# Kernel optimization log

Measured on AMD Instinct MI355X. Metric: run time of the kernel, lower is better.

## Reference

```python
import jax, jax.numpy as jnp
import numpy as np

# ---- config constants (match init_kwargs / MjModel camera params) ----
PAD_RES = (255, 255)          # padded sensor resolution (Mx, My), odd
RES = (160, 160)              # eye resolution (target_width, target_height)
APERTURE = 0.1                # aperture as fraction of sensor half-size
WAVELENGTHS = (6.1e-07, 5.3e-07, 4.7e-07)  # RGB wavelengths [m]
SENSOR_SIZE = (2e-3, 2e-3)    # (sx, sy) from MjModel.cam_sensorsize [m]


def setup_inputs() -> dict:
    key = jax.random.key(0)
    k1, k2 = jax.random.split(key)
    image = jax.random.uniform(k1, (PAD_RES[0], PAD_RES[1], 3), dtype=jnp.float32)
    depth = jax.random.uniform(k2, (PAD_RES[0], PAD_RES[1]), dtype=jnp.float32)
    return {"image": image, "depth": depth}


def _optics_consts():
    """Precompute the grids of MjCambrianOptics._reset_psf."""
    Mx, My = PAD_RES
    sx, sy = SENSOR_SIZE
    dx, dy = sx / Mx, sy / My
    Lx, Ly = dx * Mx, dy * My
    x1 = jnp.linspace(-Lx / 2.0, Lx / 2.0, Mx, dtype=jnp.float32)
    y1 = jnp.linspace(-Ly / 2.0, Ly / 2.0, My, dtype=jnp.float32)
    X1, Y1 = jnp.meshgrid(x1, y1, indexing='ij')
    fx = jnp.linspace(-1.0 / (2.0 * dx), 1.0 / (2.0 * dx), Mx, dtype=jnp.float32)
    fy = jnp.linspace(-1.0 / (2.0 * dx), 1.0 / (2.0 * dx), My, dtype=jnp.float32)  # dx for both, faithful to source
    FX, FY = jnp.meshgrid(fx, fy, indexing='ij')
    aperture_radius = min(Lx / 2, Ly / 2) * APERTURE + 1e-07
    A = (jnp.sqrt(X1**2 + Y1**2) / aperture_radius <= 1.0).astype(jnp.float32)
    wl = jnp.asarray(WAVELENGTHS, dtype=jnp.float32)[:, None, None]  # (3,1,1)
    X1_Y1 = X1**2 + Y1**2                                           # (Mx,My)
    H_valid = (jnp.sqrt(FX**2 + FY**2) < 1.0 / wl).astype(jnp.float32)  # (3,Mx,My)
    arg = 1.0 - (wl * FX) ** 2 - (wl * FY) ** 2
    # Source computes sqrt(arg) (NaN where arg<0) then nan_to_num after exp;
    # H_valid is exactly 0 where arg<=0, so clamping arg to 0 yields the same H.
    FX_FY = jnp.sqrt(jnp.maximum(arg, 0.0))                         # (3,Mx,My)
    k = (1j * 2.0 * jnp.pi / wl).astype(jnp.complex64)              # (3,1,1)
    return A, X1_Y1, H_valid, FX_FY, k


def _depth_invariant_psf(mean_depth):
    A, X1_Y1, H_valid, FX_FY, k = _optics_consts()
    # spherical wave from point source at mean_depth, masked by aperture
    u1 = jnp.exp(k * jnp.sqrt(X1_Y1 + mean_depth**2))   # (3,Mx,My) complex64
    u2 = u1 * A
    # angular-spectrum transfer function
    H = H_valid * jnp.exp(k * mean_depth * FX_FY)
    u3 = jnp.fft.ifft2(jnp.fft.fft2(H) * jnp.fft.fft2(u2))
    psf = u3 * u3                                        # complex square, faithful to torch.square
    psf = psf / (jnp.sum(psf) + 1e-07)                   # complex normalization, faithful
    return jnp.real(psf)                                 # (3,Mx,My) float32


def reference(image, depth):
    psf = _depth_invariant_psf(jnp.mean(depth))          # (3,Mx,My)
    img = jnp.transpose(image, (2, 0, 1))[None]          # (1,3,H,W)
    kern = psf[:, None].astype(img.dtype)                # (3,1,Mx,My)
    out = jax.lax.conv_general_dilated(
        img, kern, window_strides=(1, 1), padding='SAME',
        feature_group_count=3, dimension_numbers=('NCHW', 'OIHW', 'NCHW'))
    out = jnp.transpose(out[0], (1, 2, 0))               # (H,W,3)
    width, height = out.shape[0], out.shape[1]
    target_width, target_height = RES
    top = (height - target_height) // 2
    left = (width - target_width) // 2
    out = out[top:top + target_height, left:left + target_width]
    return jnp.clip(out, 0.0, 1.0)
```

## Files before the change

kernel.cpp:

```cpp
#include <hip/hip_runtime.h>
#include <hip/hip_bf16.h>
#include <math.h>


constexpr int M   = 255;
constexpr int NP  = M * M;
constexpr int RESO = 160;

constexpr int IMG_ROWS = 416, IMG_COLS = 448;
constexpr int IMG_CH   = IMG_ROWS * IMG_COLS;
constexpr int IMG_SIDE = 3 * IMG_CH;
constexpr int P4_DI   = 304 * 8;
constexpr int P4_CH   = 256 * P4_DI;
constexpr int P4_SIDE = 3 * P4_CH;

typedef __attribute__((ext_vector_type(8))) short short8;
typedef __attribute__((ext_vector_type(4))) float f32x4;

__device__ __forceinline__ unsigned short f2bf(float f) {
    unsigned int u = __float_as_uint(f);
    unsigned int r = (u + 0x7fffu + ((u >> 16) & 1u)) >> 16;
    return (unsigned short)r;
}
__device__ __forceinline__ float bf2f(unsigned short h) {
    return __uint_as_float(((unsigned int)h) << 16);
}

constexpr int MAXN = 1100;
struct PWForest {
    int kind[MAXN];
    int off[MAXN], len[MAXN];
    int li[MAXN], ri[MAXN];
    int lvl[MAXN];
    int nNode, nLeaf, maxLvl;
    int roots[16], nRoots;
};
constexpr int pwf_build(PWForest& T, int o, int n) {
    if (n <= 128) {
        int id = T.nNode++;
        T.kind[id] = 0; T.off[id] = o; T.len[id] = n;
        T.lvl[id] = 0; T.nLeaf++;
        return id;
    }
    int n2 = (n / 2) - ((n / 2) % 8);
    int a = pwf_build(T, o, n2);
    int b = pwf_build(T, o + n2, n - n2);
    int id = T.nNode++;
    T.kind[id] = 1; T.li[id] = a; T.ri[id] = b;
    int l = (T.lvl[a] > T.lvl[b] ? T.lvl[a] : T.lvl[b]) + 1;
    T.lvl[id] = l; if (l > T.maxLvl) T.maxLvl = l;
    return id;
}
constexpr PWForest pwf_make() {
    PWForest T{};
    int pos = 1, rem = NP - 1;
    while (rem > 0) {
        int c = rem > 8192 ? 8192 : rem;
        T.roots[T.nRoots++] = pwf_build(T, pos, c);
        pos += c; rem -= c;
    }
    return T;
}
constexpr PWForest PW = pwf_make();
static_assert(PW.nNode <= MAXN, "forest overflow");
static_assert(PW.nRoots == 8, "chunk count");

__global__ void k_mleaf(const float* __restrict__ depth, float* __restrict__ val) {
    int id = blockIdx.x * 256 + threadIdx.x;
    if (id >= PW.nNode || PW.kind[id] != 0) return;
    const float* a = depth + PW.off[id];
    int n = PW.len[id];
    float r0 = a[0], r1 = a[1], r2 = a[2], r3 = a[3];
    float r4 = a[4], r5 = a[5], r6 = a[6], r7 = a[7];
    int lim = n - (n % 8);
    int i = 8;
    for (; i < lim; i += 8) {
        r0 += a[i + 0]; r1 += a[i + 1]; r2 += a[i + 2]; r3 += a[i + 3];
        r4 += a[i + 4]; r5 += a[i + 5]; r6 += a[i + 6]; r7 += a[i + 7];
    }
    float res = ((r0 + r1) + (r2 + r3)) + ((r4 + r5) + (r6 + r7));
    for (; i < n; ++i) res += a[i];
    val[id] = res;
}

__global__ void k_mtree(const float* __restrict__ depth, float* __restrict__ val,
                        float* __restrict__ meanp) {
    int tid = threadIdx.x;
    for (int l = 1; l <= PW.maxLvl; ++l) {
        for (int id = tid; id < PW.nNode; id += 256)
            if (PW.kind[id] == 1 && PW.lvl[id] == l)
                val[id] = val[PW.li[id]] + val[PW.ri[id]];
        __syncthreads();
    }
    if (tid == 0) {
        float io1 = depth[0];
        for (int r = 0; r < PW.nRoots; ++r)
            io1 = io1 + val[PW.roots[r]];
        meanp[0] = io1 / 65025.0f;
    }
}

__global__ void k_prep(const float* __restrict__ img, unsigned short* __restrict__ IMG2,
                       float2* __restrict__ W,
                       float2* __restrict__ U2, float2* __restrict__ Hb,
                       const float* __restrict__ meanp,
                       double xstart, double xstep, double xstop,
                       double fstart, double fstep, double fstop,
                       float ap_f) {
#pragma clang fp contract(off)
    int idx = blockIdx.x * 256 + threadIdx.x;
    if (idx < 3 * NP) {
        int c = idx / NP, ij = idx % NP, i = ij / M, j = ij % M;
        const float wls[3] = {6.1e-07f, 5.3e-07f, 4.7e-07f};
        float wl = wls[c];
        float ki = ((float)6.283185307179586) / wl;
        float d  = meanp[0];
        float d2 = d * d;

        float x  = (i == 254) ? (float)xstop : (float)((double)i * xstep + xstart);
        float y  = (j == 254) ? (float)xstop : (float)((double)j * xstep + xstart);
        float fx = (i == 254) ? (float)fstop : (float)((double)i * fstep + fstart);
        float fy = (j == 254) ? (float)fstop : (float)((double)j * fstep + fstart);

        float xx = x * x, yy = y * y;
        float X1Y1 = xx + yy;

        float s  = sqrtf(X1Y1 + d2);
        float th = ki * s;
        float A  = (sqrtf(X1Y1) / ap_f <= 1.0f) ? 1.0f : 0.0f;
        float2 u2v;
        if (A != 0.0f) u2v = make_float2((float)cos((double)th), (float)sin((double)th));
        else           u2v = make_float2(0.0f, 0.0f);

        float a = wl * fx, b = wl * fy;
        float arg = (1.0f - a * a) - b * b;
        float FXY = sqrtf(fmaxf(arg, 0.0f));
        float Hv  = (sqrtf(fx * fx + fy * fy) < (1.0f / wl)) ? 1.0f : 0.0f;
        float kd  = ki * d;
        float ph  = kd * FXY;
        float cph = (float)cos((double)ph), sph = (float)sin((double)ph);
        float2 hv = make_float2(Hv * cph, Hv * sph);

        U2[idx] = u2v;
        Hb[idx] = hv;
        return;
    }
    if (idx < 4 * NP) {
        int e = idx - 3 * NP;
        int n = e / M, k = e % M;
        int m = (n * k) % M;
        double ang = -2.0 * 3.14159265358979323846 * (double)m / 255.0;
        W[e] = make_float2((float)cos(ang), (float)sin(ang));
        return;
    }
    int e = idx - 4 * NP;
    if (e >= IMG_SIDE) return;
    int ch = e / IMG_CH, rem = e % IMG_CH;
    int prow = rem / IMG_COLS, pcol = rem % IMG_COLS;
    int a = prow - 80, b = pcol - 80;
    float v = 0.0f;
    if (a >= 0 && a < M && b >= 0 && b < M) v = img[(a * M + b) * 3 + ch];
    unsigned short hi = f2bf(v);
    unsigned short lo = f2bf(v - bf2f(hi));
    IMG2[e] = hi;
    IMG2[IMG_SIDE + e] = lo;
}

#define CG_LOAD(KT, VA, WB0, WB1) { \
    int k0_ = (KT) * 16; \
    { int r_ = threadIdx.x >> 4, c_ = threadIdx.x & 15; \
      int gi_ = i0 + r_, gk_ = k0_ + c_; \
      VA = (gi_ < M && gk_ < M) ? Ab[gi_ * M + gk_] : make_float2(0.f, 0.f); \
      if (conjA) VA.y = -VA.y; } \
    { int r2_ = threadIdx.x >> 5, c2_ = threadIdx.x & 31; \
      int gk2_ = k0_ + r2_, gj_ = j0 + c2_; \
      WB0 = make_float2(0.f, 0.f); \
      if (gk2_ < M && gj_ < M) { \
          WB0 = Bb[gk2_ * M + gj_]; \
          if (B2b) { float2 z_ = B2b[gk2_ * M + gj_]; \
              WB0 = make_float2(WB0.x * z_.x - WB0.y * z_.y, WB0.x * z_.y + WB0.y * z_.x); } \
      } \
      if (conjB) WB0.y = -WB0.y; } \
    { int idx_ = threadIdx.x + 256; \
      int r2_ = idx_ >> 5, c2_ = idx_ & 31; \
      int gk2_ = k0_ + r2_, gj_ = j0 + c2_; \
      WB1 = make_float2(0.f, 0.f); \
      if (gk2_ < M && gj_ < M) { \
          WB1 = Bb[gk2_ * M + gj_]; \
          if (B2b) { float2 z_ = B2b[gk2_ * M + gj_]; \
              WB1 = make_float2(WB1.x * z_.x - WB1.y * z_.y, WB1.x * z_.y + WB1.y * z_.x); } \
      } \
      if (conjB) WB1.y = -WB1.y; } }

__global__ __launch_bounds__(256)
void k_cgemm(const float2* __restrict__ A, int aBatch,
             const float2* __restrict__ B, const float2* __restrict__ B2,
             int bBatch, float2* __restrict__ C,
             int conjA, int conjB, float scale) {
    __shared__ float2 As[16][17];
    __shared__ float2 Bs[16][33];
    int c = blockIdx.z;
    int tx = threadIdx.x & 15, ty = threadIdx.x >> 4;
    int i0 = blockIdx.y * 16, j0 = blockIdx.x * 32;
    const float2* Ab = A + (size_t)c * aBatch;
    const float2* Bb = B + (size_t)c * bBatch;
    const float2* B2b = B2 ? (B2 + (size_t)c * bBatch) : nullptr;
    float2 a00 = {0,0}, a01 = {0,0};

    int wrA  = threadIdx.x >> 4,  wcA  = threadIdx.x & 15;
    int wrB0 = threadIdx.x >> 5,  wcB0 = threadIdx.x & 31;
    int wrB1 = (threadIdx.x + 256) >> 5, wcB1 = (threadIdx.x + 256) & 31;

    float2 vA, wB0, wB1;
    float2 nA, nB0, nB1;
    CG_LOAD(0, vA, wB0, wB1)

    for (int kt = 0; kt < 16; ++kt) {
        As[wrA][wcA]   = vA;
        Bs[wrB0][wcB0] = wB0;
        Bs[wrB1][wcB1] = wB1;
        if (kt < 15) { CG_LOAD(kt + 1, nA, nB0, nB1) }
        __syncthreads();
#pragma unroll
        for (int kk = 0; kk < 16; ++kk) {
            float2 p = As[ty][kk];
            float2 u = Bs[kk][tx], v = Bs[kk][tx + 16];
            a00.x += p.x * u.x - p.y * u.y;  a00.y += p.x * u.y + p.y * u.x;
            a01.x += p.x * v.x - p.y * v.y;  a01.y += p.x * v.y + p.y * v.x;
        }
        __syncthreads();
        vA = nA; wB0 = nB0; wB1 = nB1;
    }
    float2* Cb = C + (size_t)c * NP;
    int gi  = i0 + ty;
    int gj0 = j0 + tx, gj1 = j0 + tx + 16;
    if (gi < M && gj0 < M) Cb[gi * M + gj0] = make_float2(a00.x * scale, a00.y * scale);
    if (gi < M && gj1 < M) Cb[gi * M + gj1] = make_float2(a01.x * scale, a01.y * scale);
}

__global__ void k_sred(const float2* __restrict__ U3, double2* __restrict__ spart) {
    __shared__ double sx[256], sy[256];
    int t = threadIdx.x;
    double ax = 0.0, ay = 0.0;
    for (int i = blockIdx.x * 256 + t; i < 3 * NP; i += 64 * 256) {
        double zx = (double)U3[i].x, zy = (double)U3[i].y;
        ax += zx * zx - zy * zy;
        ay += 2.0 * zx * zy;
    }
    sx[t] = ax; sy[t] = ay;
    __syncthreads();
    for (int w = 128; w > 0; w >>= 1) {
        if (t < w) { sx[t] += sx[t + w]; sy[t] += sy[t + w]; }
        __syncthreads();
    }
    if (t == 0) spart[blockIdx.x] = make_double2(sx[0], sy[0]);
}

__global__ void k_sfin(const double2* __restrict__ spart, double* __restrict__ sfin) {
    if (threadIdx.x != 0 || blockIdx.x != 0) return;
    double rx = 0.0, ry = 0.0;
    for (int i = 0; i < 64; ++i) { rx += spart[i].x; ry += spart[i].y; }
    double dsx = rx + 1e-7, dsy = ry;
    sfin[0] = dsx;
    sfin[1] = dsy;
    sfin[2] = 1.0 / (dsx * dsx + dsy * dsy);
}

__global__ void k_p4(const float2* __restrict__ U3, const double* __restrict__ sfin,
                     unsigned short* __restrict__ P4) {
    int idx = blockIdx.x * 256 + threadIdx.x;
    if (idx >= P4_SIDE) return;
    double dsx = sfin[0], dsy = sfin[1], inv = sfin[2];
    int ch = idx / P4_CH, rem = idx % P4_CH;
    int di = rem / P4_DI, rem2 = rem % P4_DI;
    int u = rem2 / 8, t = rem2 % 8;
    int p = u - 16 + t;
    float v = 0.0f;
    if (di < M && p >= 0 && p < M) {
        float2 zf = U3[(ch * M + di) * M + p];
        double zx = (double)zf.x, zy = (double)zf.y;
        double zr = zx * zx - zy * zy;
        double zi = 2.0 * zx * zy;
        v = (float)((zr * dsx + zi * dsy) * inv);
    }
    unsigned short hi = f2bf(v);
    unsigned short lo = f2bf(v - bf2f(hi));
    P4[idx] = hi;
    P4[P4_SIDE + idx] = lo;
}

constexpr int LDS_STRIDE = 312;

#define SB __builtin_amdgcn_sched_barrier(0);

#define REP9(OP) OP(0) OP(1) OP(2) OP(3) OP(4) OP(5) OP(6) OP(7) OP(8)

#define DECLA(i) short8 Ah_##i, Al_##i;
#define DECLB(i) short8 Bh_##i, Bl_##i;

#define LDA(i) Ah_##i = *(const short8*)(prH + 256 * i); \
               Al_##i = *(const short8*)(prL + 256 * i);
#define LDB(i) Bh_##i = *(const short8*)(prH + 256 * i); \
               Bl_##i = *(const short8*)(prL + 256 * i);
#define LOADA(dl) { const unsigned short* prH = pHc + (size_t)(d0 + (dl)) * P4_DI + aoff; \
                    const unsigned short* prL = pLc + (size_t)(d0 + (dl)) * P4_DI + aoff; \
                    REP9(LDA) }
#define LOADB(dl) { const unsigned short* prH = pHc + (size_t)(d0 + (dl)) * P4_DI + aoff; \
                    const unsigned short* prL = pLc + (size_t)(d0 + (dl)) * P4_DI + aoff; \
                    REP9(LDB) }

#define CMA(i) { \
    short8 bh0 = *(const short8*)&ldsI[0][rrow][32 * i + 8 * q]; \
    short8 bl0 = *(const short8*)&ldsI[1][rrow][32 * i + 8 * q]; \
    short8 bh1 = *(const short8*)&ldsI[0][rrow][32 * i + 8 * q + 16]; \
    short8 bl1 = *(const short8*)&ldsI[1][rrow][32 * i + 8 * q + 16]; \
    aHH0 = __builtin_amdgcn_mfma_f32_16x16x32_bf16(Ah_##i, bh0, aHH0, 0, 0, 0); \
    aHL0 = __builtin_amdgcn_mfma_f32_16x16x32_bf16(Ah_##i, bl0, aHL0, 0, 0, 0); \
    aLH0 = __builtin_amdgcn_mfma_f32_16x16x32_bf16(Al_##i, bh0, aLH0, 0, 0, 0); \
    aHH1 = __builtin_amdgcn_mfma_f32_16x16x32_bf16(Ah_##i, bh1, aHH1, 0, 0, 0); \
    aHL1 = __builtin_amdgcn_mfma_f32_16x16x32_bf16(Ah_##i, bl1, aHL1, 0, 0, 0); \
    aLH1 = __builtin_amdgcn_mfma_f32_16x16x32_bf16(Al_##i, bh1, aLH1, 0, 0, 0); }
#define CMB(i) { \
    short8 bh0 = *(const short8*)&ldsI[0][rrow][32 * i + 8 * q]; \
    short8 bl0 = *(const short8*)&ldsI[1][rrow][32 * i + 8 * q]; \
    short8 bh1 = *(const short8*)&ldsI[0][rrow][32 * i + 8 * q + 16]; \
    short8 bl1 = *(const short8*)&ldsI[1][rrow][32 * i + 8 * q + 16]; \
    aHH0 = __builtin_amdgcn_mfma_f32_16x16x32_bf16(Bh_##i, bh0, aHH0, 0, 0, 0); \
    aHL0 = __builtin_amdgcn_mfma_f32_16x16x32_bf16(Bh_##i, bl0, aHL0, 0, 0, 0); \
    aLH0 = __builtin_amdgcn_mfma_f32_16x16x32_bf16(Bl_##i, bh0, aLH0, 0, 0, 0); \
    aHH1 = __builtin_amdgcn_mfma_f32_16x16x32_bf16(Bh_##i, bh1, aHH1, 0, 0, 0); \
    aHL1 = __builtin_amdgcn_mfma_f32_16x16x32_bf16(Bh_##i, bl1, aHL1, 0, 0, 0); \
    aLH1 = __builtin_amdgcn_mfma_f32_16x16x32_bf16(Bl_##i, bh1, aLH1, 0, 0, 0); }
#define COMPA(dl) { int rrow = ln + (dl); REP9(CMA) }
#define COMPB(dl) { int rrow = ln + (dl); REP9(CMB) }

__global__ __launch_bounds__(256, 2)
void k_conv(const unsigned short* __restrict__ IMG2,
            const unsigned short* __restrict__ P4,
            float* __restrict__ PART) {
    __shared__ __align__(16) unsigned short ldsI[2][31][LDS_STRIDE];

    int tid  = threadIdx.x;
    int w    = tid >> 6;
    int lane = tid & 63;
    int ln   = lane & 15;
    int q    = lane >> 4;
    int j0 = blockIdx.x * 32;
    int i0 = blockIdx.y * 16;
    int bz = blockIdx.z;
    int ch = bz >> 4, chunk = bz & 15;
    int d0 = chunk << 4;

    const unsigned short* imgH = IMG2 + ch * IMG_CH;
    const unsigned short* imgL = imgH + IMG_SIDE;
    const unsigned short* pHc  = P4 + ch * P4_CH;
    const unsigned short* pLc  = pHc + P4_SIDE;

    int su0  = 16 + 8 * q - ln;
    int aoff = su0 * 8;

    f32x4 aHH0 = {0.f,0.f,0.f,0.f}, aHL0 = {0.f,0.f,0.f,0.f}, aLH0 = {0.f,0.f,0.f,0.f};
    f32x4 aHH1 = {0.f,0.f,0.f,0.f}, aHL1 = {0.f,0.f,0.f,0.f}, aLH1 = {0.f,0.f,0.f,0.f};

    REP9(DECLA)
    REP9(DECLB)

    int dbase = 4 * w;
    LOADA(dbase + 0)

    int row0 = i0 + d0;
    for (int idx = tid; idx < 2 * 31 * 38; idx += 256) {
        int plane = idx / (31 * 38);
        int rem = idx - plane * (31 * 38);
        int r = rem / 38, c = rem - r * 38;
        const unsigned short* src =
            (plane ? imgL : imgH) + (size_t)(row0 + r) * IMG_COLS + j0 + c * 8;
        *(short8*)&ldsI[plane][r][c * 8] = *(const short8*)src;
    }
    __syncthreads();

    LOADB(dbase + 1)
    SB
    COMPA(dbase + 0)
    SB
    LOADA(dbase + 2)
    SB
    COMPB(dbase + 1)
    SB
    LOADB(dbase + 3)
    SB
    COMPA(dbase + 2)
    SB
    COMPB(dbase + 3)

    f32x4 tot0, tot1;
#pragma unroll
    for (int r = 0; r < 4; ++r) {
        tot0[r] = aHH0[r] + aHL0[r] + aLH0[r];
        tot1[r] = aHH1[r] + aHL1[r] + aLH1[r];
    }

    __syncthreads();
    float* red = (float*)&ldsI[0][0][0];
    if (w) {
#pragma unroll
        for (int r = 0; r < 4; ++r) {
            red[((w - 1) * 64 + lane) * 8 + r]     = tot0[r];
            red[((w - 1) * 64 + lane) * 8 + 4 + r] = tot1[r];
        }
    }
    __syncthreads();
    if (w == 0) {
#pragma unroll
        for (int wv = 0; wv < 3; ++wv)
#pragma unroll
            for (int r = 0; r < 4; ++r) {
                tot0[r] += red[(wv * 64 + lane) * 8 + r];
                tot1[r] += red[(wv * 64 + lane) * 8 + 4 + r];
            }
        float* op = PART + (size_t)bz * (RESO * RESO) + (i0 + ln) * RESO + j0 + 4 * q;
        float4 o0; o0.x = tot0[0]; o0.y = tot0[1]; o0.z = tot0[2]; o0.w = tot0[3];
        float4 o1; o1.x = tot1[0]; o1.y = tot1[1]; o1.z = tot1[2]; o1.w = tot1[3];
        *(float4*)op = o0;
        *(float4*)(op + 16) = o1;
    }
}

__global__ void k_out(const float* __restrict__ PART, float* __restrict__ out) {
    int idx = blockIdx.x * 256 + threadIdx.x;
    if (idx >= 3 * RESO * RESO) return;
    int c = idx / (RESO * RESO), ij = idx % (RESO * RESO);
    float s = 0.0f;
    for (int kz = 0; kz < 16; ++kz)
        s += PART[(size_t)(c * 16 + kz) * (RESO * RESO) + ij];
    s = fminf(fmaxf(s, 0.0f), 1.0f);
    int i = ij / RESO, j = ij % RESO;
    out[(i * RESO + j) * 3 + c] = s;
}

extern "C" void kernel_launch(void* const* d_in, const int* in_sizes, int n_in,
                              void* d_out, int out_size, void* d_ws, size_t ws_size,
                              hipStream_t stream) {
    const float* image = (const float*)d_in[0];
    const float* depth = (const float*)d_in[1];
    float* out = (float*)d_out;

    char* p = (char*)d_ws;
    auto alloc = [&](size_t bytes) { void* r = (void*)p; p += (bytes + 255) & ~(size_t)255; return r; };
    float*   meanp = (float*)alloc(4);
    float*   mval  = (float*)alloc(MAXN * 4);
    double*  sfin  = (double*)alloc(3 * 8);
    float2*  Wf    = (float2*)alloc((size_t)NP * 8);
    float2*  UH    = (float2*)alloc((size_t)6 * NP * 8);
    float2*  Td    = (float2*)alloc((size_t)6 * NP * 8);
    float2*  EF    = (float2*)alloc((size_t)6 * NP * 8);
    float2*  U3    = (float2*)alloc((size_t)3 * NP * 8);
    double2* spart = (double2*)alloc(64 * 16);
    unsigned short* P4   = (unsigned short*)alloc((size_t)2 * P4_SIDE * 2);
    unsigned short* IMG2 = (unsigned short*)alloc((size_t)2 * IMG_SIDE * 2);
    float*   PART  = (float*)alloc((size_t)48 * RESO * RESO * 4);

    float2* U2 = UH;
    float2* Hb = UH + (size_t)3 * NP;

    double dx = 0.002 / 255.0;
    double Lx = dx * 255.0;
    double ap = (Lx / 2.0) * 0.1 + 1e-7;
    float ap_f = (float)ap;

    double xstart = -(Lx / 2.0);
    double xstop  =  Lx / 2.0;
    double xstep  = (xstop - xstart) / 254.0;
    double fstart = -1.0 / (2.0 * dx);
    double fstop  =  1.0 / (2.0 * dx);
    double fstep  = (fstop - fstart) / 254.0;

    k_mleaf<<<(PW.nNode + 255) / 256, 256, 0, stream>>>(depth, mval);
    k_mtree<<<1, 256, 0, stream>>>(depth, mval, meanp);
    int gprep = (4 * NP + IMG_SIDE + 255) / 256;
    k_prep<<<gprep, 256, 0, stream>>>(image, IMG2, Wf, U2, Hb, meanp,
                                      xstart, xstep, xstop,
                                      fstart, fstep, fstop, ap_f);

    dim3 bb(256);
    k_cgemm<<<dim3(8, 16, 6), bb, 0, stream>>>(Wf, 0, UH, nullptr, NP, Td, 0, 0, 1.0f);
    k_cgemm<<<dim3(8, 16, 6), bb, 0, stream>>>(Td, NP, Wf, nullptr, 0, EF, 0, 0, 1.0f);
    k_cgemm<<<dim3(8, 16, 3), bb, 0, stream>>>(Wf, 0, EF + (size_t)3 * NP, EF, NP,
                                               Td, 1, 0, 1.0f / 255.0f);
    k_cgemm<<<dim3(8, 16, 3), bb, 0, stream>>>(Td, NP, Wf, nullptr, 0, U3, 0, 1,
                                               1.0f / 255.0f);

    k_sred<<<64, 256, 0, stream>>>(U3, spart);
    k_sfin<<<1, 64, 0, stream>>>(spart, sfin);
    k_p4<<<(P4_SIDE + 255) / 256, 256, 0, stream>>>(U3, sfin, P4);

    k_conv<<<dim3(5, 10, 48), 256, 0, stream>>>(IMG2, P4, PART);
    k_out<<<300, 256, 0, stream>>>(PART, out);
}
```

Measured before the change: 252.7 us.

## Double conv output rows per block to reuse PSF A-fragments; fold sfin into k_p4

The convolution block now computes 32 output rows instead of 16, so each PSF fragment held in registers feeds twice as many MFMAs. This halves the P4 global loads per output and halves the grid in y, at the cost of more accumulator registers and a taller LDS image tile. Separately, the single-thread k_sfin kernel is removed: every k_p4 block now re-reduces the 64 partial sums in shared memory, trading a kernel launch for redundant tiny work per block.

```diff
diff --git a/kernel.cpp b/kernel.cpp
--- a/kernel.cpp
+++ b/kernel.cpp
@@ -256,21 +256,20 @@
     if (t == 0) spart[blockIdx.x] = make_double2(sx[0], sy[0]);
 }
 
-__global__ void k_sfin(const double2* __restrict__ spart, double* __restrict__ sfin) {
-    if (threadIdx.x != 0 || blockIdx.x != 0) return;
-    double rx = 0.0, ry = 0.0;
-    for (int i = 0; i < 64; ++i) { rx += spart[i].x; ry += spart[i].y; }
-    double dsx = rx + 1e-7, dsy = ry;
-    sfin[0] = dsx;
-    sfin[1] = dsy;
-    sfin[2] = 1.0 / (dsx * dsx + dsy * dsy);
-}
-
-__global__ void k_p4(const float2* __restrict__ U3, const double* __restrict__ sfin,
+__global__ void k_p4(const float2* __restrict__ U3, const double2* __restrict__ spart,
                      unsigned short* __restrict__ P4) {
+    __shared__ double sh[3];
+    if (threadIdx.x == 0) {
+        double rx = 0.0, ry = 0.0;
+        for (int i = 0; i < 64; ++i) { rx += spart[i].x; ry += spart[i].y; }
+        double dsx_ = rx + 1e-7, dsy_ = ry;
+        sh[0] = dsx_; sh[1] = dsy_;
+        sh[2] = 1.0 / (dsx_ * dsx_ + dsy_ * dsy_);
+    }
+    __syncthreads();
     int idx = blockIdx.x * 256 + threadIdx.x;
     if (idx >= P4_SIDE) return;
-    double dsx = sfin[0], dsy = sfin[1], inv = sfin[2];
+    double dsx = sh[0], dsy = sh[1], inv = sh[2];
     int ch = idx / P4_CH, rem = idx % P4_CH;
     int di = rem / P4_DI, rem2 = rem % P4_DI;
     int u = rem2 / 8, t = rem2 % 8;
@@ -309,28 +308,30 @@
                     const unsigned short* prL = pLc + (size_t)(d0 + (dl)) * P4_DI + aoff; \
                     REP9(LDB) }
 
-#define CMA(i) { \
-    short8 bh0 = *(const short8*)&ldsI[0][rrow][32 * i + 8 * q]; \
-    short8 bl0 = *(const short8*)&ldsI[1][rrow][32 * i + 8 * q]; \
-    short8 bh1 = *(const short8*)&ldsI[0][rrow][32 * i + 8 * q + 16]; \
-    short8 bl1 = *(const short8*)&ldsI[1][rrow][32 * i + 8 * q + 16]; \
-    aHH0 = __builtin_amdgcn_mfma_f32_16x16x32_bf16(Ah_##i, bh0, aHH0, 0, 0, 0); \
-    aHL0 = __builtin_amdgcn_mfma_f32_16x16x32_bf16(Ah_##i, bl0, aHL0, 0, 0, 0); \
-    aLH0 = __builtin_amdgcn_mfma_f32_16x16x32_bf16(Al_##i, bh0, aLH0, 0, 0, 0); \
-    aHH1 = __builtin_amdgcn_mfma_f32_16x16x32_bf16(Ah_##i, bh1, aHH1, 0, 0, 0); \
-    aHL1 = __builtin_amdgcn_mfma_f32_16x16x32_bf16(Ah_##i, bl1, aHL1, 0, 0, 0); \
-    aLH1 = __builtin_amdgcn_mfma_f32_16x16x32_bf16(Al_##i, bh1, aLH1, 0, 0, 0); }
-#define CMB(i) { \
-    short8 bh0 = *(const short8*)&ldsI[0][rrow][32 * i + 8 * q]; \
-    short8 bl0 = *(const short8*)&ldsI[1][rrow][32 * i + 8 * q]; \
-    short8 bh1 = *(const short8*)&ldsI[0][rrow][32 * i + 8 * q + 16]; \
-    short8 bl1 = *(const short8*)&ldsI[1][rrow][32 * i + 8 * q + 16]; \
-    aHH0 = __builtin_amdgcn_mfma_f32_16x16x32_bf16(Bh_##i, bh0, aHH0, 0, 0, 0); \
-    aHL0 = __builtin_amdgcn_mfma_f32_16x16x32_bf16(Bh_##i, bl0, aHL0, 0, 0, 0); \
-    aLH0 = __builtin_amdgcn_mfma_f32_16x16x32_bf16(Bl_##i, bh0, aLH0, 0, 0, 0); \
-    aHH1 = __builtin_amdgcn_mfma_f32_16x16x32_bf16(Bh_##i, bh1, aHH1, 0, 0, 0); \
-    aHL1 = __builtin_amdgcn_mfma_f32_16x16x32_bf16(Bh_##i, bl1, aHL1, 0, 0, 0); \
-    aLH1 = __builtin_amdgcn_mfma_f32_16x16x32_bf16(Bl_##i, bh1, aLH1, 0, 0, 0); }
+#define CMBODY(AH, AL) { \
+    short8 bh00 = *(const short8*)&ldsI[0][rrow][colb]; \
+    short8 bl00 = *(const short8*)&ldsI[1][rrow][colb]; \
+    short8 bh01 = *(const short8*)&ldsI[0][rrow][colb + 16]; \
+    short8 bl01 = *(const short8*)&ldsI[1][rrow][colb + 16]; \
+    short8 bh10 = *(const short8*)&ldsI[0][rrow + 16][colb]; \
+    short8 bl10 = *(const short8*)&ldsI[1][rrow + 16][colb]; \
+    short8 bh11 = *(const short8*)&ldsI[0][rrow + 16][colb + 16]; \
+    short8 bl11 = *(const short8*)&ldsI[1][rrow + 16][colb + 16]; \
+    aHH00 = __builtin_amdgcn_mfma_f32_16x16x32_bf16(AH, bh00, aHH00, 0, 0, 0); \
+    aHL00 = __builtin_amdgcn_mfma_f32_16x16x32_bf16(AH, bl00, aHL00, 0, 0, 0); \
+    aLH00 = __builtin_amdgcn_mfma_f32_16x16x32_bf16(AL, bh00, aLH00, 0, 0, 0); \
+    aHH01 = __builtin_amdgcn_mfma_f32_16x16x32_bf16(AH, bh01, aHH01, 0, 0, 0); \
+    aHL01 = __builtin_amdgcn_mfma_f32_16x16x32_bf16(AH, bl01, aHL01, 0, 0, 0); \
+    aLH01 = __builtin_amdgcn_mfma_f32_16x16x32_bf16(AL, bh01, aLH01, 0, 0, 0); \
+    aHH10 = __builtin_amdgcn_mfma_f32_16x16x32_bf16(AH, bh10, aHH10, 0, 0, 0); \
+    aHL10 = __builtin_amdgcn_mfma_f32_16x16x32_bf16(AH, bl10, aHL10, 0, 0, 0); \
+    aLH10 = __builtin_amdgcn_mfma_f32_16x16x32_bf16(AL, bh10, aLH10, 0, 0, 0); \
+    aHH11 = __builtin_amdgcn_mfma_f32_16x16x32_bf16(AH, bh11, aHH11, 0, 0, 0); \
+    aHL11 = __builtin_amdgcn_mfma_f32_16x16x32_bf16(AH, bl11, aHL11, 0, 0, 0); \
+    aLH11 = __builtin_amdgcn_mfma_f32_16x16x32_bf16(AL, bh11, aLH11, 0, 0, 0); }
+
+#define CMA(i) { int colb = 32 * i + 8 * q; CMBODY(Ah_##i, Al_##i) }
+#define CMB(i) { int colb = 32 * i + 8 * q; CMBODY(Bh_##i, Bl_##i) }
 #define COMPA(dl) { int rrow = ln + (dl); REP9(CMA) }
 #define COMPB(dl) { int rrow = ln + (dl); REP9(CMB) }
 
@@ -338,7 +339,7 @@
 void k_conv(const unsigned short* __restrict__ IMG2,
             const unsigned short* __restrict__ P4,
             float* __restrict__ PART) {
-    __shared__ __align__(16) unsigned short ldsI[2][31][LDS_STRIDE];
+    __shared__ __align__(16) unsigned short ldsI[2][47][LDS_STRIDE];
 
     int tid  = threadIdx.x;
     int w    = tid >> 6;
@@ -346,7 +347,7 @@
     int ln   = lane & 15;
     int q    = lane >> 4;
     int j0 = blockIdx.x * 32;
-    int i0 = blockIdx.y * 16;
+    int i0 = blockIdx.y * 32;
     int bz = blockIdx.z;
     int ch = bz >> 4, chunk = bz & 15;
     int d0 = chunk << 4;
@@ -359,8 +360,10 @@
     int su0  = 16 + 8 * q - ln;
     int aoff = su0 * 8;
 
-    f32x4 aHH0 = {0.f,0.f,0.f,0.f}, aHL0 = {0.f,0.f,0.f,0.f}, aLH0 = {0.f,0.f,0.f,0.f};
-    f32x4 aHH1 = {0.f,0.f,0.f,0.f}, aHL1 = {0.f,0.f,0.f,0.f}, aLH1 = {0.f,0.f,0.f,0.f};
+    f32x4 aHH00 = {0,0,0,0}, aHL00 = {0,0,0,0}, aLH00 = {0,0,0,0};
+    f32x4 aHH01 = {0,0,0,0}, aHL01 = {0,0,0,0}, aLH01 = {0,0,0,0};
+    f32x4 aHH10 = {0,0,0,0}, aHL10 = {0,0,0,0}, aLH10 = {0,0,0,0};
+    f32x4 aHH11 = {0,0,0,0}, aHL11 = {0,0,0,0}, aLH11 = {0,0,0,0};
 
     REP9(DECLA)
     REP9(DECLB)
@@ -369,9 +372,9 @@
     LOADA(dbase + 0)
 
     int row0 = i0 + d0;
-    for (int idx = tid; idx < 2 * 31 * 38; idx += 256) {
-        int plane = idx / (31 * 38);
-        int rem = idx - plane * (31 * 38);
+    for (int idx = tid; idx < 2 * 47 * 38; idx += 256) {
+        int plane = idx / (47 * 38);
+        int rem = idx - plane * (47 * 38);
         int r = rem / 38, c = rem - r * 38;
         const unsigned short* src =
             (plane ? imgL : imgH) + (size_t)(row0 + r) * IMG_COLS + j0 + c * 8;
@@ -393,11 +396,13 @@
     SB
     COMPB(dbase + 3)
 
-    f32x4 tot0, tot1;
+    f32x4 tot00, tot01, tot10, tot11;
 #pragma unroll
     for (int r = 0; r < 4; ++r) {
-        tot0[r] = aHH0[r] + aHL0[r] + aLH0[r];
-        tot1[r] = aHH1[r] + aHL1[r] + aLH1[r];
+        tot00[r] = aHH00[r] + aHL00[r] + aLH00[r];
+        tot01[r] = aHH01[r] + aHL01[r] + aLH01[r];
+        tot10[r] = aHH10[r] + aHL10[r] + aLH10[r];
+        tot11[r] = aHH11[r] + aHL11[r] + aLH11[r];
     }
 
     __syncthreads();
@@ -405,8 +410,11 @@
     if (w) {
 #pragma unroll
         for (int r = 0; r < 4; ++r) {
-            red[((w - 1) * 64 + lane) * 8 + r]     = tot0[r];
-            red[((w - 1) * 64 + lane) * 8 + 4 + r] = tot1[r];
+            int base = ((w - 1) * 64 + lane) * 16;
+            red[base + r]      = tot00[r];
+            red[base + 4 + r]  = tot01[r];
+            red[base + 8 + r]  = tot10[r];
+            red[base + 12 + r] = tot11[r];
         }
     }
     __syncthreads();
@@ -415,14 +423,23 @@
         for (int wv = 0; wv < 3; ++wv)
 #pragma unroll
             for (int r = 0; r < 4; ++r) {
-                tot0[r] += red[(wv * 64 + lane) * 8 + r];
-                tot1[r] += red[(wv * 64 + lane) * 8 + 4 + r];
+                int base = (wv * 64 + lane) * 16;
+                tot00[r] += red[base + r];
+                tot01[r] += red[base + 4 + r];
+                tot10[r] += red[base + 8 + r];
+                tot11[r] += red[base + 12 + r];
             }
-        float* op = PART + (size_t)bz * (RESO * RESO) + (i0 + ln) * RESO + j0 + 4 * q;
-        float4 o0; o0.x = tot0[0]; o0.y = tot0[1]; o0.z = tot0[2]; o0.w = tot0[3];
-        float4 o1; o1.x = tot1[0]; o1.y = tot1[1]; o1.z = tot1[2]; o1.w = tot1[3];
-        *(float4*)op = o0;
-        *(float4*)(op + 16) = o1;
+        float* op0 = PART + (size_t)bz * (RESO * RESO) + (i0 + ln) * RESO + j0 + 4 * q;
+        float* op1 = PART + (size_t)bz * (RESO * RESO) + (i0 + 16 + ln) * RESO + j0 + 4 * q;
+        float4 o;
+        o.x = tot00[0]; o.y = tot00[1]; o.z = tot00[2]; o.w = tot00[3];
+        *(float4*)op0 = o;
+        o.x = tot01[0]; o.y = tot01[1]; o.z = tot01[2]; o.w = tot01[3];
+        *(float4*)(op0 + 16) = o;
+        o.x = tot10[0]; o.y = tot10[1]; o.z = tot10[2]; o.w = tot10[3];
+        *(float4*)op1 = o;
+        o.x = tot11[0]; o.y = tot11[1]; o.z = tot11[2]; o.w = tot11[3];
+        *(float4*)(op1 + 16) = o;
     }
 }
 
@@ -449,7 +466,6 @@
     auto alloc = [&](size_t bytes) { void* r = (void*)p; p += (bytes + 255) & ~(size_t)255; return r; };
     float*   meanp = (float*)alloc(4);
     float*   mval  = (float*)alloc(MAXN * 4);
-    double*  sfin  = (double*)alloc(3 * 8);
     float2*  Wf    = (float2*)alloc((size_t)NP * 8);
     float2*  UH    = (float2*)alloc((size_t)6 * NP * 8);
     float2*  Td    = (float2*)alloc((size_t)6 * NP * 8);
@@ -491,9 +507,8 @@
                                                1.0f / 255.0f);
 
     k_sred<<<64, 256, 0, stream>>>(U3, spart);
-    k_sfin<<<1, 64, 0, stream>>>(spart, sfin);
-    k_p4<<<(P4_SIDE + 255) / 256, 256, 0, stream>>>(U3, sfin, P4);
-
-    k_conv<<<dim3(5, 10, 48), 256, 0, stream>>>(IMG2, P4, PART);
+    k_p4<<<(P4_SIDE + 255) / 256, 256, 0, stream>>>(U3, spart, P4);
+
+    k_conv<<<dim3(5, 5, 48), 256, 0, stream>>>(IMG2, P4, PART);
     k_out<<<300, 256, 0, stream>>>(PART, out);
 }
```

After: 249.6 us. No clear change (-1.2%).
